# Performance work log

Hardware: AMD Instinct MI355X
Metric: run time of the kernel (lower is better)

## Reference

```python
import jax, jax.numpy as jnp
import numpy as np

N_NODES = 100000
N_EDGES = 1600000
IN_DIM, HID_DIM, OUT_DIM = 128, 128, 64


def setup_inputs() -> dict:
    key = jax.random.key(0)
    k1, k2, k3, k4 = jax.random.split(key, 4)
    x = jax.random.normal(k1, (N_NODES, IN_DIM), dtype=jnp.float32)
    edge_index = jax.random.randint(k2, (2, N_EDGES), 0, N_NODES, dtype=jnp.int64)
    W1 = jax.random.normal(k3, (IN_DIM, HID_DIM), dtype=jnp.float32) * (1.0 / np.sqrt(IN_DIM))
    b1 = jnp.zeros((HID_DIM,), dtype=jnp.float32)
    W2 = jax.random.normal(k4, (HID_DIM, OUT_DIM), dtype=jnp.float32) * (1.0 / np.sqrt(HID_DIM))
    b2 = jnp.zeros((OUT_DIM,), dtype=jnp.float32)
    return {"x": x, "edge_index": edge_index, "W1": W1, "b1": b1, "W2": W2, "b2": b2}


def _gcn_conv(x, W, b, src, dst, num_nodes):
    # PyG GCNConv (normalize=True): h = D^{-1/2} A_hat D^{-1/2} (x W) + b
    h = x @ W  # [N, out]
    ones = jnp.ones(src.shape[0], dtype=h.dtype)
    deg = jax.ops.segment_sum(ones, dst, num_segments=num_nodes)  # in-degree incl self-loops
    dinv = jnp.where(deg > 0, jax.lax.rsqrt(deg), jnp.zeros_like(deg))
    norm = dinv[src] * dinv[dst]  # [E]
    msg = h[src] * norm[:, None]  # gather + scale, [E, out]
    out = jax.ops.segment_sum(msg, dst, num_segments=num_nodes)  # scatter-add
    return out + b


def reference(x, edge_index, W1, b1, W2, b2):
    n = x.shape[0]
    loop = jnp.arange(n, dtype=edge_index.dtype)
    src = jnp.concatenate([edge_index[0], loop])  # add_self_loops=True
    dst = jnp.concatenate([edge_index[1], loop])
    h = jax.nn.elu(_gcn_conv(x, W1, b1, src, dst, n))
    out = jax.nn.elu(_gcn_conv(h, W2, b2, src, dst, n))
    return out
```

## Files before the change

kernel.cpp:

```cpp
#include <hip/hip_runtime.h>
#include <hip/hip_bf16.h>

#define N_NODES 100000
#define N_EDGES 1600000
#define IN_DIM  128
#define HID_DIM 128
#define OUT_DIM 64

#define BKT_BITS 9
#define BKT_SIZE 512
#define NBUCK    ((N_NODES + BKT_SIZE - 1) / BKT_SIZE)
#define BCAP     9024
#define EPB      8192

typedef __attribute__((ext_vector_type(8))) short short8;
typedef __attribute__((ext_vector_type(4))) float floatx4;

__device__ __forceinline__ float eluf(float x) { return x > 0.0f ? x : expm1f(x); }
__device__ __forceinline__ unsigned short bfbits(float f) {
    union { __hip_bfloat16 h; unsigned short u; } c; c.h = __float2bfloat16(f); return c.u;
}
__device__ __forceinline__ unsigned packbf(float a, float b) {
    return (unsigned)bfbits(a) | ((unsigned)bfbits(b) << 16);
}
__device__ __forceinline__ float lo16(unsigned u) { return __uint_as_float(u << 16); }
__device__ __forceinline__ float hi16(unsigned u) { return __uint_as_float(u & 0xffff0000u); }
__device__ __forceinline__ float dinv_of(int deg) { return rsqrtf((float)deg + 1.0f); }

__global__ void k_detect(const int* __restrict__ ei, int* __restrict__ flag,
                         int* __restrict__ cursor) {
    __shared__ int acc;
    if (threadIdx.x == 0) acc = 0;
    __syncthreads();
    int v = 0;
    for (int e = threadIdx.x; e < 1024; e += 256) v |= ei[2 * e + 1];
    atomicOr(&acc, v);
    __syncthreads();
    if (threadIdx.x == 0) flag[0] = (acc == 0) ? 1 : 0;
    if (threadIdx.x < NBUCK) cursor[threadIdx.x] = threadIdx.x * BCAP;
}
__device__ __forceinline__ int esrc(const int* ei, int e, int is64) {
    return is64 ? ei[2 * e] : ei[e];
}
__device__ __forceinline__ int edst(const int* ei, int e, int is64) {
    return is64 ? ei[2 * (N_EDGES + e)] : ei[N_EDGES + e];
}

__launch_bounds__(256)
__global__ void k_bucket(const int* __restrict__ ei, const int* __restrict__ flag,
                         int* __restrict__ cursor, unsigned* __restrict__ eb) {
    __shared__ int hist[NBUCK];
    __shared__ int base[NBUCK];
    int t = threadIdx.x;
    int is64 = flag[0];
    int e0 = blockIdx.x * EPB;
    for (int i = t; i < NBUCK; i += 256) hist[i] = 0;
    __syncthreads();
    for (int i = t; i < EPB; i += 256) {
        int e = e0 + i;
        if (e >= N_EDGES) break;
        int d = edst(ei, e, is64);
        atomicAdd(&hist[d >> BKT_BITS], 1);
    }
    __syncthreads();
    for (int i = t; i < NBUCK; i += 256)
        base[i] = atomicAdd(&cursor[i], hist[i]);
    __syncthreads();
    for (int i = t; i < EPB; i += 256) {
        int e = e0 + i;
        if (e >= N_EDGES) break;
        int d = edst(ei, e, is64);
        int s = esrc(ei, e, is64);
        int bk = d >> BKT_BITS;
        int p = atomicAdd(&base[bk], 1);
        if (p < (bk + 1) * BCAP)
            eb[p] = ((unsigned)s << BKT_BITS) | (unsigned)(d & (BKT_SIZE - 1));
    }
}

__launch_bounds__(256)
__global__ void k_csr(const int* __restrict__ cursor, unsigned* __restrict__ eb,
                      int* __restrict__ rowStart, unsigned char* __restrict__ deg8) {
    __shared__ unsigned stage[BCAP];
    __shared__ int hist[BKT_SIZE];
    __shared__ int excl[BKT_SIZE];
    __shared__ int cur[BKT_SIZE];
    __shared__ int sc[256];
    int t = threadIdx.x, b = blockIdx.x;
    int cbeg = b * BCAP;
    int count = cursor[b] - cbeg;
    if (count > BCAP) count = BCAP;
    for (int i = t; i < BKT_SIZE; i += 256) hist[i] = 0;
    __syncthreads();
    for (int i = t; i < count; i += 256) {
        unsigned e = eb[cbeg + i];
        stage[i] = e;
        atomicAdd(&hist[e & (BKT_SIZE - 1)], 1);
    }
    __syncthreads();
    int h0 = hist[2 * t], h1 = hist[2 * t + 1];
    int s = h0 + h1;
    sc[t] = s;
    __syncthreads();
    int acc = s;
    for (int off = 1; off < 256; off <<= 1) {
        int v = (t >= off) ? sc[t - off] : 0;
        __syncthreads();
        acc += v; sc[t] = acc;
        __syncthreads();
    }
    int ex = acc - s;
    excl[2 * t] = ex;       excl[2 * t + 1] = ex + h0;
    cur[2 * t] = ex;        cur[2 * t + 1] = ex + h0;
    int nbase = b * BKT_SIZE;
    for (int i = t; i < BKT_SIZE; i += 256) {
        int n = nbase + i;
        if (n < N_NODES) {
            rowStart[n] = cbeg + excl[i];
            deg8[n] = (unsigned char)hist[i];
        }
    }
    __syncthreads();
    for (int i = t; i < count; i += 256) {
        unsigned e = stage[i];
        int p = atomicAdd(&cur[e & (BKT_SIZE - 1)], 1);
        eb[cbeg + p] = e >> BKT_BITS;
    }
}

__global__ void k_cast_x(const float4* __restrict__ x4, uint2* __restrict__ xb) {
    int i = blockIdx.x * blockDim.x + threadIdx.x;
    if (i >= N_NODES * (IN_DIM / 4)) return;
    float4 v = x4[i];
    uint2 o = { packbf(v.x, v.y), packbf(v.z, v.w) };
    xb[i] = o;
}

__launch_bounds__(256)
__global__ void k_gather1(const unsigned* __restrict__ xb, const unsigned char* __restrict__ deg8,
                          const int* __restrict__ row, const unsigned* __restrict__ csr,
                          unsigned* __restrict__ agg) {
    int w = (blockIdx.x * blockDim.x + threadIdx.x) >> 6;
    int lane = threadIdx.x & 63;
    if (w >= N_NODES) return;
    int beg = row[w];
    int dg = deg8[w];
    int end = beg + dg;
    float dd = dinv_of(dg);
    unsigned sv = xb[w * 64 + lane];
    float ax = lo16(sv) * dd, ay = hi16(sv) * dd;
    int j = beg;
    for (; j + 8 <= end; j += 8) {
        int s[8]; float wd[8]; unsigned u[8];
#pragma unroll
        for (int q = 0; q < 8; q++) s[q] = (int)csr[j + q];
#pragma unroll
        for (int q = 0; q < 8; q++) wd[q] = dinv_of(deg8[s[q]]);
#pragma unroll
        for (int q = 0; q < 8; q++) u[q] = xb[s[q] * 64 + lane];
#pragma unroll
        for (int q = 0; q < 8; q++) { ax += lo16(u[q]) * wd[q]; ay += hi16(u[q]) * wd[q]; }
    }
    for (; j + 2 <= end; j += 2) {
        int s0 = (int)csr[j], s1 = (int)csr[j + 1];
        float w0 = dinv_of(deg8[s0]), w1 = dinv_of(deg8[s1]);
        unsigned u0 = xb[s0 * 64 + lane];
        unsigned u1 = xb[s1 * 64 + lane];
        ax += lo16(u0) * w0 + lo16(u1) * w1;
        ay += hi16(u0) * w0 + hi16(u1) * w1;
    }
    if (j < end) {
        int s0 = (int)csr[j]; float w0 = dinv_of(deg8[s0]);
        unsigned u0 = xb[s0 * 64 + lane];
        ax += lo16(u0) * w0; ay += hi16(u0) * w0;
    }
    agg[w * 64 + lane] = packbf(ax * dd, ay * dd);
}

__launch_bounds__(256)
__global__ void k_gather2(const unsigned* __restrict__ h2, const unsigned char* __restrict__ deg8,
                          const int* __restrict__ row, const unsigned* __restrict__ csr,
                          const float* __restrict__ b2, float* __restrict__ out) {
    int w = (blockIdx.x * blockDim.x + threadIdx.x) >> 5;
    int p = threadIdx.x & 31;
    if (w >= N_NODES) return;
    float2 bias = *(const float2*)(b2 + 2 * p);
    int beg = row[w];
    int dg = deg8[w];
    int end = beg + dg;
    float dd = dinv_of(dg);
    unsigned sv = h2[w * 32 + p];
    float ax = lo16(sv) * dd, ay = hi16(sv) * dd;
    int j = beg;
    for (; j + 8 <= end; j += 8) {
        int s[8]; float wd[8]; unsigned u[8];
#pragma unroll
        for (int q = 0; q < 8; q++) s[q] = (int)csr[j + q];
#pragma unroll
        for (int q = 0; q < 8; q++) wd[q] = dinv_of(deg8[s[q]]);
#pragma unroll
        for (int q = 0; q < 8; q++) u[q] = h2[s[q] * 32 + p];
#pragma unroll
        for (int q = 0; q < 8; q++) { ax += lo16(u[q]) * wd[q]; ay += hi16(u[q]) * wd[q]; }
    }
    for (; j + 2 <= end; j += 2) {
        int s0 = (int)csr[j], s1 = (int)csr[j + 1];
        float w0 = dinv_of(deg8[s0]), w1 = dinv_of(deg8[s1]);
        unsigned u0 = h2[s0 * 32 + p];
        unsigned u1 = h2[s1 * 32 + p];
        ax += lo16(u0) * w0 + lo16(u1) * w1;
        ay += hi16(u0) * w0 + hi16(u1) * w1;
    }
    if (j < end) {
        int s0 = (int)csr[j]; float w0 = dinv_of(deg8[s0]);
        unsigned u0 = h2[s0 * 32 + p];
        ax += lo16(u0) * w0; ay += hi16(u0) * w0;
    }
    ax *= dd; ay *= dd;
    float2 r = { eluf(ax + bias.x), eluf(ay + bias.y) };
    *(float2*)(out + w * OUT_DIM + 2 * p) = r;
}

__launch_bounds__(256)
__global__ void k_gemm1_mfma(unsigned* __restrict__ agg, const float* __restrict__ W1,
                             const float* __restrict__ b1, int nblk) {
    __shared__ short w1p[4][8][64][8];
    int t = threadIdx.x;
    for (int idx = t; idx < 8192; idx += 256) {
        int j2 = idx & 3, l = (idx >> 2) & 63, ct = (idx >> 8) & 7, kk = idx >> 11;
        int k = kk * 32 + (l >> 4) * 8 + j2 * 2;
        int c = ct * 16 + (l & 15);
        ((unsigned*)w1p)[idx] = packbf(W1[k * HID_DIM + c], W1[(k + 1) * HID_DIM + c]);
    }
    int lane = t & 63, wave = t >> 6;
    int q = lane >> 4, m = lane & 15;
    floatx4 bias[8];
#pragma unroll
    for (int ct = 0; ct < 8; ct++) bias[ct] = *(const floatx4*)(b1 + ct * 16 + q * 4);
    __syncthreads();
    for (int blk = blockIdx.x * 4 + wave; blk < nblk; blk += gridDim.x * 4) {
        int r = blk * 16 + m;
        const short8* arow = (const short8*)(agg + r * 64);
        short8 bfr[4];
#pragma unroll
        for (int kk = 0; kk < 4; kk++) bfr[kk] = arow[kk * 4 + q];
        floatx4 acc[8];
#pragma unroll
        for (int ct = 0; ct < 8; ct++) acc[ct] = (floatx4)0.0f;
#pragma unroll
        for (int kk = 0; kk < 4; kk++)
#pragma unroll
            for (int ct = 0; ct < 8; ct++) {
                short8 af = *(const short8*)(&w1p[kk][ct][lane][0]);
                acc[ct] = __builtin_amdgcn_mfma_f32_16x16x32_bf16(af, bfr[kk], acc[ct], 0, 0, 0);
            }
        unsigned* hrow = agg + r * 64;
#pragma unroll
        for (int ct = 0; ct < 8; ct++) {
            uint2 o;
            o.x = packbf(eluf(acc[ct][0] + bias[ct][0]), eluf(acc[ct][1] + bias[ct][1]));
            o.y = packbf(eluf(acc[ct][2] + bias[ct][2]), eluf(acc[ct][3] + bias[ct][3]));
            *(uint2*)(hrow + ct * 8 + q * 2) = o;
        }
    }
}

__launch_bounds__(256)
__global__ void k_gemm2_mfma(const unsigned* __restrict__ h1, const float* __restrict__ W2,
                             unsigned* __restrict__ h2, int nblk) {
    __shared__ short w2p[4][4][64][8];
    int t = threadIdx.x;
    for (int idx = t; idx < 4096; idx += 256) {
        int j2 = idx & 3, l = (idx >> 2) & 63, ct = (idx >> 8) & 3, kk = idx >> 10;
        int k = kk * 32 + (l >> 4) * 8 + j2 * 2;
        int c = ct * 16 + (l & 15);
        ((unsigned*)w2p)[idx] = packbf(W2[k * OUT_DIM + c], W2[(k + 1) * OUT_DIM + c]);
    }
    int lane = t & 63, wave = t >> 6;
    int q = lane >> 4, m = lane & 15;
    __syncthreads();
    for (int blk = blockIdx.x * 4 + wave; blk < nblk; blk += gridDim.x * 4) {
        int r = blk * 16 + m;
        const short8* arow = (const short8*)(h1 + r * 64);
        short8 bfr[4];
#pragma unroll
        for (int kk = 0; kk < 4; kk++) bfr[kk] = arow[kk * 4 + q];
        floatx4 acc[4];
#pragma unroll
        for (int ct = 0; ct < 4; ct++) acc[ct] = (floatx4)0.0f;
#pragma unroll
        for (int kk = 0; kk < 4; kk++)
#pragma unroll
            for (int ct = 0; ct < 4; ct++) {
                short8 af = *(const short8*)(&w2p[kk][ct][lane][0]);
                acc[ct] = __builtin_amdgcn_mfma_f32_16x16x32_bf16(af, bfr[kk], acc[ct], 0, 0, 0);
            }
        unsigned* orow = h2 + r * 32;
#pragma unroll
        for (int ct = 0; ct < 4; ct++) {
            uint2 o;
            o.x = packbf(acc[ct][0], acc[ct][1]);
            o.y = packbf(acc[ct][2], acc[ct][3]);
            *(uint2*)(orow + ct * 8 + q * 2) = o;
        }
    }
}

extern "C" void kernel_launch(void* const* d_in, const int* in_sizes, int n_in,
                              void* d_out, int out_size, void* d_ws, size_t ws_size,
                              hipStream_t stream) {
    const float* x  = (const float*)d_in[0];
    const int*   ei = (const int*)d_in[1];
    const float* W1 = (const float*)d_in[2];
    const float* b1 = (const float*)d_in[3];
    const float* W2 = (const float*)d_in[4];
    const float* b2 = (const float*)d_in[5];

    const size_t OFF_FLAG = 0;
    const size_t OFF_CUR  = 16;
    const size_t OFF_ROW  = 272;
    const size_t OFF_DEG8 = 100272;
    const size_t OFF_EB   = 125272;
    const size_t OFF_XB   = 1893976;
    const size_t OFF_AGG  = 8293976;
    const size_t needed = (OFF_AGG + 6400000) * 4;
    if (ws_size < needed) return;

    int*           flag   = (int*)d_ws + OFF_FLAG;
    int*           cursor = (int*)d_ws + OFF_CUR;
    int*           row    = (int*)d_ws + OFF_ROW;
    unsigned char* deg8   = (unsigned char*)((int*)d_ws + OFF_DEG8);
    unsigned*      eb     = (unsigned*)d_ws + OFF_EB;
    unsigned*      xb     = (unsigned*)d_ws + OFF_XB;
    unsigned*      agg    = (unsigned*)d_ws + OFF_AGG;

    k_detect<<<1, 256, 0, stream>>>(ei, flag, cursor);
    k_bucket<<<(N_EDGES + EPB - 1) / EPB, 256, 0, stream>>>(ei, flag, cursor, eb);
    k_csr<<<NBUCK, 256, 0, stream>>>(cursor, eb, row, deg8);

    k_cast_x<<<(N_NODES * (IN_DIM / 4) + 255) / 256, 256, 0, stream>>>(
        (const float4*)x, (uint2*)xb);

    k_gather1<<<(N_NODES * 64 + 255) / 256, 256, 0, stream>>>(xb, deg8, row, eb, agg);
    k_gemm1_mfma<<<1024, 256, 0, stream>>>(agg, W1, b1, N_NODES / 16);

    k_gemm2_mfma<<<1024, 256, 0, stream>>>(agg, W2, xb, N_NODES / 16);
    k_gather2<<<(N_NODES * 32 + 255) / 256, 256, 0, stream>>>(
        xb, deg8, row, eb, b2, (float*)d_out);
}
```

Baseline: 332.3 us.

## Fuse cast into CSR build, precompute dinv, widen gather loads, shrink bucket blocks

The x-to-bf16 cast moves into extra blocks of the CSR build kernel, which removes one launch. The CSR build now stores a per-node dinv array and 16-bit row offsets, so the gathers read dinv directly instead of recomputing rsqrt from deg8. Both gather kernels switch to 8-byte loads per lane, with half as many lanes per node, to cut the number of load instructions in the hot loop. The bucket kernel now caches edges in registers, uses smaller blocks and relative cursors, and skips atomics for empty buckets; BCAP shrinks, which raises the risk of overflowing a bucket.

```diff
diff --git a/kernel.cpp b/kernel.cpp
--- a/kernel.cpp
+++ b/kernel.cpp
@@ -10,8 +10,9 @@
 #define BKT_BITS 9
 #define BKT_SIZE 512
 #define NBUCK    ((N_NODES + BKT_SIZE - 1) / BKT_SIZE)
-#define BCAP     9024
-#define EPB      8192
+#define BCAP     8768
+#define EPB      2048
+#define CAST_BLKS 3125
 
 typedef __attribute__((ext_vector_type(8))) short short8;
 typedef __attribute__((ext_vector_type(4))) float floatx4;
@@ -25,10 +26,16 @@
 }
 __device__ __forceinline__ float lo16(unsigned u) { return __uint_as_float(u << 16); }
 __device__ __forceinline__ float hi16(unsigned u) { return __uint_as_float(u & 0xffff0000u); }
-__device__ __forceinline__ float dinv_of(int deg) { return rsqrtf((float)deg + 1.0f); }
-
-__global__ void k_detect(const int* __restrict__ ei, int* __restrict__ flag,
-                         int* __restrict__ cursor) {
+
+__device__ __forceinline__ int esrc(const int* ei, int e, int is64) {
+    return is64 ? ei[2 * e] : ei[e];
+}
+__device__ __forceinline__ int edst(const int* ei, int e, int is64) {
+    return is64 ? ei[2 * (N_EDGES + e)] : ei[N_EDGES + e];
+}
+
+__global__ void k_init(const int* __restrict__ ei, int* __restrict__ flag,
+                       int* __restrict__ cursor) {
     __shared__ int acc;
     if (threadIdx.x == 0) acc = 0;
     __syncthreads();
@@ -37,13 +44,7 @@
     atomicOr(&acc, v);
     __syncthreads();
     if (threadIdx.x == 0) flag[0] = (acc == 0) ? 1 : 0;
-    if (threadIdx.x < NBUCK) cursor[threadIdx.x] = threadIdx.x * BCAP;
-}
-__device__ __forceinline__ int esrc(const int* ei, int e, int is64) {
-    return is64 ? ei[2 * e] : ei[e];
-}
-__device__ __forceinline__ int edst(const int* ei, int e, int is64) {
-    return is64 ? ei[2 * (N_EDGES + e)] : ei[N_EDGES + e];
+    if (threadIdx.x < NBUCK) cursor[threadIdx.x] = 0;
 }
 
 __launch_bounds__(256)
@@ -54,41 +55,60 @@
     int t = threadIdx.x;
     int is64 = flag[0];
     int e0 = blockIdx.x * EPB;
+    int s[8], d[8];
+#pragma unroll
+    for (int q = 0; q < 8; q++) {
+        int e = e0 + q * 256 + t;
+        if (e < N_EDGES) { s[q] = esrc(ei, e, is64); d[q] = edst(ei, e, is64); }
+        else d[q] = -1;
+    }
     for (int i = t; i < NBUCK; i += 256) hist[i] = 0;
     __syncthreads();
-    for (int i = t; i < EPB; i += 256) {
-        int e = e0 + i;
-        if (e >= N_EDGES) break;
-        int d = edst(ei, e, is64);
-        atomicAdd(&hist[d >> BKT_BITS], 1);
-    }
-    __syncthreads();
-    for (int i = t; i < NBUCK; i += 256)
-        base[i] = atomicAdd(&cursor[i], hist[i]);
-    __syncthreads();
-    for (int i = t; i < EPB; i += 256) {
-        int e = e0 + i;
-        if (e >= N_EDGES) break;
-        int d = edst(ei, e, is64);
-        int s = esrc(ei, e, is64);
-        int bk = d >> BKT_BITS;
-        int p = atomicAdd(&base[bk], 1);
-        if (p < (bk + 1) * BCAP)
-            eb[p] = ((unsigned)s << BKT_BITS) | (unsigned)(d & (BKT_SIZE - 1));
-    }
-}
-
-__launch_bounds__(256)
-__global__ void k_csr(const int* __restrict__ cursor, unsigned* __restrict__ eb,
-                      int* __restrict__ rowStart, unsigned char* __restrict__ deg8) {
+#pragma unroll
+    for (int q = 0; q < 8; q++)
+        if (d[q] >= 0) atomicAdd(&hist[d[q] >> BKT_BITS], 1);
+    __syncthreads();
+    for (int i = t; i < NBUCK; i += 256) {
+        int h = hist[i];
+        base[i] = (h > 0) ? atomicAdd(&cursor[i], h) : 0;
+    }
+    __syncthreads();
+#pragma unroll
+    for (int q = 0; q < 8; q++)
+        if (d[q] >= 0) {
+            int bk = d[q] >> BKT_BITS;
+            int p = atomicAdd(&base[bk], 1);
+            if (p < BCAP)
+                eb[bk * BCAP + p] = ((unsigned)s[q] << BKT_BITS) | (unsigned)(d[q] & (BKT_SIZE - 1));
+        }
+}
+
+__launch_bounds__(256)
+__global__ void k_csr_cast(const int* __restrict__ cursor, unsigned* __restrict__ eb,
+                           unsigned short* __restrict__ row16, unsigned char* __restrict__ deg8,
+                           float* __restrict__ dinv,
+                           const float4* __restrict__ x4, uint2* __restrict__ xb) {
     __shared__ unsigned stage[BCAP];
     __shared__ int hist[BKT_SIZE];
     __shared__ int excl[BKT_SIZE];
     __shared__ int cur[BKT_SIZE];
     __shared__ int sc[256];
     int t = threadIdx.x, b = blockIdx.x;
+    if (b >= NBUCK) {
+        int i0 = (b - NBUCK) * 1024 + t;
+#pragma unroll
+        for (int q = 0; q < 4; q++) {
+            int i = i0 + q * 256;
+            if (i < N_NODES * (IN_DIM / 4)) {
+                float4 v = x4[i];
+                uint2 o = { packbf(v.x, v.y), packbf(v.z, v.w) };
+                xb[i] = o;
+            }
+        }
+        return;
+    }
     int cbeg = b * BCAP;
-    int count = cursor[b] - cbeg;
+    int count = cursor[b];
     if (count > BCAP) count = BCAP;
     for (int i = t; i < BKT_SIZE; i += 256) hist[i] = 0;
     __syncthreads();
@@ -116,8 +136,9 @@
     for (int i = t; i < BKT_SIZE; i += 256) {
         int n = nbase + i;
         if (n < N_NODES) {
-            rowStart[n] = cbeg + excl[i];
+            row16[n] = (unsigned short)excl[i];
             deg8[n] = (unsigned char)hist[i];
+            dinv[n] = rsqrtf((float)hist[i] + 1.0f);
         }
     }
     __syncthreads();
@@ -128,97 +149,101 @@
     }
 }
 
-__global__ void k_cast_x(const float4* __restrict__ x4, uint2* __restrict__ xb) {
-    int i = blockIdx.x * blockDim.x + threadIdx.x;
-    if (i >= N_NODES * (IN_DIM / 4)) return;
-    float4 v = x4[i];
-    uint2 o = { packbf(v.x, v.y), packbf(v.z, v.w) };
-    xb[i] = o;
-}
-
-__launch_bounds__(256)
-__global__ void k_gather1(const unsigned* __restrict__ xb, const unsigned char* __restrict__ deg8,
-                          const int* __restrict__ row, const unsigned* __restrict__ csr,
-                          unsigned* __restrict__ agg) {
-    int w = (blockIdx.x * blockDim.x + threadIdx.x) >> 6;
-    int lane = threadIdx.x & 63;
-    if (w >= N_NODES) return;
-    int beg = row[w];
-    int dg = deg8[w];
-    int end = beg + dg;
-    float dd = dinv_of(dg);
-    unsigned sv = xb[w * 64 + lane];
-    float ax = lo16(sv) * dd, ay = hi16(sv) * dd;
-    int j = beg;
-    for (; j + 8 <= end; j += 8) {
-        int s[8]; float wd[8]; unsigned u[8];
-#pragma unroll
-        for (int q = 0; q < 8; q++) s[q] = (int)csr[j + q];
-#pragma unroll
-        for (int q = 0; q < 8; q++) wd[q] = dinv_of(deg8[s[q]]);
-#pragma unroll
-        for (int q = 0; q < 8; q++) u[q] = xb[s[q] * 64 + lane];
-#pragma unroll
-        for (int q = 0; q < 8; q++) { ax += lo16(u[q]) * wd[q]; ay += hi16(u[q]) * wd[q]; }
-    }
-    for (; j + 2 <= end; j += 2) {
-        int s0 = (int)csr[j], s1 = (int)csr[j + 1];
-        float w0 = dinv_of(deg8[s0]), w1 = dinv_of(deg8[s1]);
-        unsigned u0 = xb[s0 * 64 + lane];
-        unsigned u1 = xb[s1 * 64 + lane];
-        ax += lo16(u0) * w0 + lo16(u1) * w1;
-        ay += hi16(u0) * w0 + hi16(u1) * w1;
-    }
-    if (j < end) {
-        int s0 = (int)csr[j]; float w0 = dinv_of(deg8[s0]);
-        unsigned u0 = xb[s0 * 64 + lane];
-        ax += lo16(u0) * w0; ay += hi16(u0) * w0;
-    }
-    agg[w * 64 + lane] = packbf(ax * dd, ay * dd);
-}
-
-__launch_bounds__(256)
-__global__ void k_gather2(const unsigned* __restrict__ h2, const unsigned char* __restrict__ deg8,
-                          const int* __restrict__ row, const unsigned* __restrict__ csr,
-                          const float* __restrict__ b2, float* __restrict__ out) {
+__launch_bounds__(256)
+__global__ void k_gather1(const uint2* __restrict__ xb2, const float* __restrict__ dinv,
+                          const unsigned short* __restrict__ row16,
+                          const unsigned char* __restrict__ deg8,
+                          const unsigned* __restrict__ csr, uint2* __restrict__ agg2) {
     int w = (blockIdx.x * blockDim.x + threadIdx.x) >> 5;
     int p = threadIdx.x & 31;
     if (w >= N_NODES) return;
-    float2 bias = *(const float2*)(b2 + 2 * p);
-    int beg = row[w];
-    int dg = deg8[w];
-    int end = beg + dg;
-    float dd = dinv_of(dg);
-    unsigned sv = h2[w * 32 + p];
-    float ax = lo16(sv) * dd, ay = hi16(sv) * dd;
+    int beg = (w >> BKT_BITS) * BCAP + row16[w];
+    int end = beg + deg8[w];
+    float dd = dinv[w];
+    uint2 sv = xb2[w * 32 + p];
+    float a0 = lo16(sv.x) * dd, a1 = hi16(sv.x) * dd;
+    float a2 = lo16(sv.y) * dd, a3 = hi16(sv.y) * dd;
     int j = beg;
     for (; j + 8 <= end; j += 8) {
-        int s[8]; float wd[8]; unsigned u[8];
+        int s[8]; float wd[8]; uint2 u[8];
 #pragma unroll
         for (int q = 0; q < 8; q++) s[q] = (int)csr[j + q];
 #pragma unroll
-        for (int q = 0; q < 8; q++) wd[q] = dinv_of(deg8[s[q]]);
-#pragma unroll
-        for (int q = 0; q < 8; q++) u[q] = h2[s[q] * 32 + p];
-#pragma unroll
-        for (int q = 0; q < 8; q++) { ax += lo16(u[q]) * wd[q]; ay += hi16(u[q]) * wd[q]; }
+        for (int q = 0; q < 8; q++) wd[q] = dinv[s[q]];
+#pragma unroll
+        for (int q = 0; q < 8; q++) u[q] = xb2[s[q] * 32 + p];
+#pragma unroll
+        for (int q = 0; q < 8; q++) {
+            a0 += lo16(u[q].x) * wd[q]; a1 += hi16(u[q].x) * wd[q];
+            a2 += lo16(u[q].y) * wd[q]; a3 += hi16(u[q].y) * wd[q];
+        }
     }
     for (; j + 2 <= end; j += 2) {
         int s0 = (int)csr[j], s1 = (int)csr[j + 1];
-        float w0 = dinv_of(deg8[s0]), w1 = dinv_of(deg8[s1]);
-        unsigned u0 = h2[s0 * 32 + p];
-        unsigned u1 = h2[s1 * 32 + p];
-        ax += lo16(u0) * w0 + lo16(u1) * w1;
-        ay += hi16(u0) * w0 + hi16(u1) * w1;
+        float w0 = dinv[s0], w1 = dinv[s1];
+        uint2 u0 = xb2[s0 * 32 + p];
+        uint2 u1 = xb2[s1 * 32 + p];
+        a0 += lo16(u0.x) * w0 + lo16(u1.x) * w1; a1 += hi16(u0.x) * w0 + hi16(u1.x) * w1;
+        a2 += lo16(u0.y) * w0 + lo16(u1.y) * w1; a3 += hi16(u0.y) * w0 + hi16(u1.y) * w1;
     }
     if (j < end) {
-        int s0 = (int)csr[j]; float w0 = dinv_of(deg8[s0]);
-        unsigned u0 = h2[s0 * 32 + p];
-        ax += lo16(u0) * w0; ay += hi16(u0) * w0;
-    }
-    ax *= dd; ay *= dd;
-    float2 r = { eluf(ax + bias.x), eluf(ay + bias.y) };
-    *(float2*)(out + w * OUT_DIM + 2 * p) = r;
+        int s0 = (int)csr[j]; float w0 = dinv[s0];
+        uint2 u0 = xb2[s0 * 32 + p];
+        a0 += lo16(u0.x) * w0; a1 += hi16(u0.x) * w0;
+        a2 += lo16(u0.y) * w0; a3 += hi16(u0.y) * w0;
+    }
+    uint2 o = { packbf(a0 * dd, a1 * dd), packbf(a2 * dd, a3 * dd) };
+    agg2[w * 32 + p] = o;
+}
+
+__launch_bounds__(256)
+__global__ void k_gather2(const uint2* __restrict__ h2, const float* __restrict__ dinv,
+                          const unsigned short* __restrict__ row16,
+                          const unsigned char* __restrict__ deg8,
+                          const unsigned* __restrict__ csr,
+                          const float* __restrict__ b2, float4* __restrict__ out) {
+    int w = (blockIdx.x * blockDim.x + threadIdx.x) >> 4;
+    int p = threadIdx.x & 15;
+    if (w >= N_NODES) return;
+    float4 bias = *(const float4*)(b2 + 4 * p);
+    int beg = (w >> BKT_BITS) * BCAP + row16[w];
+    int end = beg + deg8[w];
+    float dd = dinv[w];
+    uint2 sv = h2[w * 16 + p];
+    float a0 = lo16(sv.x) * dd, a1 = hi16(sv.x) * dd;
+    float a2 = lo16(sv.y) * dd, a3 = hi16(sv.y) * dd;
+    int j = beg;
+    for (; j + 8 <= end; j += 8) {
+        int s[8]; float wd[8]; uint2 u[8];
+#pragma unroll
+        for (int q = 0; q < 8; q++) s[q] = (int)csr[j + q];
+#pragma unroll
+        for (int q = 0; q < 8; q++) wd[q] = dinv[s[q]];
+#pragma unroll
+        for (int q = 0; q < 8; q++) u[q] = h2[s[q] * 16 + p];
+#pragma unroll
+        for (int q = 0; q < 8; q++) {
+            a0 += lo16(u[q].x) * wd[q]; a1 += hi16(u[q].x) * wd[q];
+            a2 += lo16(u[q].y) * wd[q]; a3 += hi16(u[q].y) * wd[q];
+        }
+    }
+    for (; j + 2 <= end; j += 2) {
+        int s0 = (int)csr[j], s1 = (int)csr[j + 1];
+        float w0 = dinv[s0], w1 = dinv[s1];
+        uint2 u0 = h2[s0 * 16 + p];
+        uint2 u1 = h2[s1 * 16 + p];
+        a0 += lo16(u0.x) * w0 + lo16(u1.x) * w1; a1 += hi16(u0.x) * w0 + hi16(u1.x) * w1;
+        a2 += lo16(u0.y) * w0 + lo16(u1.y) * w1; a3 += hi16(u0.y) * w0 + hi16(u1.y) * w1;
+    }
+    if (j < end) {
+        int s0 = (int)csr[j]; float w0 = dinv[s0];
+        uint2 u0 = h2[s0 * 16 + p];
+        a0 += lo16(u0.x) * w0; a1 += hi16(u0.x) * w0;
+        a2 += lo16(u0.y) * w0; a3 += hi16(u0.y) * w0;
+    }
+    a0 *= dd; a1 *= dd; a2 *= dd; a3 *= dd;
+    float4 r = { eluf(a0 + bias.x), eluf(a1 + bias.y), eluf(a2 + bias.z), eluf(a3 + bias.w) };
+    out[w * 16 + p] = r;
 }
 
 __launch_bounds__(256)
@@ -316,35 +341,36 @@
     const float* W2 = (const float*)d_in[4];
     const float* b2 = (const float*)d_in[5];
 
-    const size_t OFF_FLAG = 0;
-    const size_t OFF_CUR  = 16;
-    const size_t OFF_ROW  = 272;
-    const size_t OFF_DEG8 = 100272;
-    const size_t OFF_EB   = 125272;
-    const size_t OFF_XB   = 1893976;
-    const size_t OFF_AGG  = 8293976;
+    const size_t OFF_FLAG  = 0;
+    const size_t OFF_CUR   = 16;
+    const size_t OFF_ROW16 = 272;
+    const size_t OFF_DEG8  = 50272;
+    const size_t OFF_DINV  = 75272;
+    const size_t OFF_EB    = 175272;
+    const size_t OFF_XB    = 1893800;
+    const size_t OFF_AGG   = 8293800;
     const size_t needed = (OFF_AGG + 6400000) * 4;
     if (ws_size < needed) return;
 
-    int*           flag   = (int*)d_ws + OFF_FLAG;
-    int*           cursor = (int*)d_ws + OFF_CUR;
-    int*           row    = (int*)d_ws + OFF_ROW;
-    unsigned char* deg8   = (unsigned char*)((int*)d_ws + OFF_DEG8);
-    unsigned*      eb     = (unsigned*)d_ws + OFF_EB;
-    unsigned*      xb     = (unsigned*)d_ws + OFF_XB;
-    unsigned*      agg    = (unsigned*)d_ws + OFF_AGG;
-
-    k_detect<<<1, 256, 0, stream>>>(ei, flag, cursor);
+    int*            flag   = (int*)d_ws + OFF_FLAG;
+    int*            cursor = (int*)d_ws + OFF_CUR;
+    unsigned short* row16  = (unsigned short*)((int*)d_ws + OFF_ROW16);
+    unsigned char*  deg8   = (unsigned char*)((int*)d_ws + OFF_DEG8);
+    float*          dinv   = (float*)d_ws + OFF_DINV;
+    unsigned*       eb     = (unsigned*)d_ws + OFF_EB;
+    unsigned*       xb     = (unsigned*)d_ws + OFF_XB;
+    unsigned*       agg    = (unsigned*)d_ws + OFF_AGG;
+
+    k_init<<<1, 256, 0, stream>>>(ei, flag, cursor);
     k_bucket<<<(N_EDGES + EPB - 1) / EPB, 256, 0, stream>>>(ei, flag, cursor, eb);
-    k_csr<<<NBUCK, 256, 0, stream>>>(cursor, eb, row, deg8);
-
-    k_cast_x<<<(N_NODES * (IN_DIM / 4) + 255) / 256, 256, 0, stream>>>(
-        (const float4*)x, (uint2*)xb);
-
-    k_gather1<<<(N_NODES * 64 + 255) / 256, 256, 0, stream>>>(xb, deg8, row, eb, agg);
+    k_csr_cast<<<NBUCK + CAST_BLKS, 256, 0, stream>>>(cursor, eb, row16, deg8, dinv,
+                                                      (const float4*)x, (uint2*)xb);
+
+    k_gather1<<<(N_NODES * 32 + 255) / 256, 256, 0, stream>>>(
+        (const uint2*)xb, dinv, row16, deg8, eb, (uint2*)agg);
     k_gemm1_mfma<<<1024, 256, 0, stream>>>(agg, W1, b1, N_NODES / 16);
 
     k_gemm2_mfma<<<1024, 256, 0, stream>>>(agg, W2, xb, N_NODES / 16);
-    k_gather2<<<(N_NODES * 32 + 255) / 256, 256, 0, stream>>>(
-        xb, deg8, row, eb, b2, (float*)d_out);
-}
+    k_gather2<<<(N_NODES * 16 + 255) / 256, 256, 0, stream>>>(
+        (const uint2*)xb, dinv, row16, deg8, eb, b2, (float4*)d_out);
+}
```

Measured after the change: 326.9 us. No clear change (-1.6%).
